# Kernel optimization log

Measured on AMD Instinct MI355X. Metric: run time of the kernel, lower is better.

Reference implementation:

```python
import jax, jax.numpy as jnp
import numpy as np

B, T, V, E, H = 64, 64, 32000, 512, 1024


def setup_inputs() -> dict:
    key = jax.random.key(0)
    ks = jax.random.split(key, 12)
    s = 0.02
    return {
        "hidden": jax.random.normal(ks[0], (2, B, H), jnp.float32),
        "cell": jax.random.normal(ks[1], (2, B, H), jnp.float32),
        "captions": jax.random.randint(ks[2], (B, T), 0, V, jnp.int32),
        "embed_W": jax.random.normal(ks[3], (V, E), jnp.float32) * s,
        "W_ih0": jax.random.normal(ks[4], (4 * H, E), jnp.float32) * s,
        "W_hh0": jax.random.normal(ks[5], (4 * H, H), jnp.float32) * s,
        "b_ih0": jnp.zeros((4 * H,), jnp.float32),
        "b_hh0": jnp.zeros((4 * H,), jnp.float32),
        "W_ih1": jax.random.normal(ks[6], (4 * H, H), jnp.float32) * s,
        "W_hh1": jax.random.normal(ks[7], (4 * H, H), jnp.float32) * s,
        "b_ih1": jnp.zeros((4 * H,), jnp.float32),
        "b_hh1": jnp.zeros((4 * H,), jnp.float32),
        "Wp_voc": jax.random.normal(ks[8], (V, H), jnp.float32) * s,
        "bp_voc": jnp.zeros((V,), jnp.float32),
    }


def lstm_cell(x, h, c, W_ih, W_hh, b):
    # PyTorch gate order: input, forget, cell(g), output
    gates = x @ W_ih.T + h @ W_hh.T + b  # [B, 4H]
    i, f, g, o = jnp.split(gates, 4, axis=-1)
    i, f, o = jax.nn.sigmoid(i), jax.nn.sigmoid(f), jax.nn.sigmoid(o)
    g = jnp.tanh(g)
    c_new = f * c + i * g
    h_new = o * jnp.tanh(c_new)
    return h_new, c_new


def reference(hidden, cell, captions, embed_W, W_ih0, W_hh0, b_ih0, b_hh0,
              W_ih1, W_hh1, b_ih1, b_hh1, Wp_voc, bp_voc):
    # teacher forcing (ratio=1.0): LSTM input at step t is embed(captions[:, t-1])
    x_seq = embed_W[captions[:, :-1]]        # [B, T-1, E]
    x_seq = jnp.swapaxes(x_seq, 0, 1)        # [T-1, B, E] time-major for scan
    b0 = b_ih0 + b_hh0
    b1 = b_ih1 + b_hh1

    def step(carry, x):
        h0, c0, h1, c1 = carry
        h0, c0 = lstm_cell(x, h0, c0, W_ih0, W_hh0, b0)
        h1, c1 = lstm_cell(h0, h1, c1, W_ih1, W_hh1, b1)
        logits = h1 @ Wp_voc.T + bp_voc      # [B, V]
        return (h0, c0, h1, c1), logits

    carry = (hidden[0], cell[0], hidden[1], cell[1])
    _, logits = jax.lax.scan(step, carry, x_seq)   # [T-1, B, V]
    logits = jnp.swapaxes(logits, 0, 1)            # [B, T-1, V]
    # outputs[:, 0, :] stays zero as in the torch code
    return jnp.concatenate([jnp.zeros((logits.shape[0], 1, logits.shape[2]), logits.dtype), logits], axis=1)
```

## Files before the change

kernel.cpp:

```cpp
#include <hip/hip_runtime.h>

#define B_    64
#define T_    64
#define V_    32000
#define E_    512
#define H_    1024
#define G4_   4096
#define TS_   63
#define MROWS 4032
#define MPAD  4096
#define BH    (B_ * H_)
#define FPAD  32

typedef __attribute__((ext_vector_type(8))) short bf16x8;
typedef __attribute__((ext_vector_type(4))) float f32x4;
typedef __attribute__((ext_vector_type(4))) unsigned int uint32x4;

__device__ __forceinline__ unsigned short bfbits(float f) {
  union { float f; unsigned int u; } cv; cv.f = f;
  unsigned int u = cv.u;
  u += 0x7fffu + ((u >> 16) & 1u);
  return (unsigned short)(u >> 16);
}
__device__ __forceinline__ float bf2f(unsigned short h) {
  union { unsigned int u; float f; } cv; cv.u = ((unsigned int)h) << 16;
  return cv.f;
}
__device__ __forceinline__ float fsig(float x) { return 1.f / (1.f + __expf(-x)); }
__device__ __forceinline__ float ftanh(float x) {
  x = fminf(fmaxf(x, -10.f), 10.f);
  const float e = __expf(2.f * x);
  return (e - 1.f) / (e + 1.f);
}

__device__ __forceinline__ void store_dword_dc(void* p, unsigned int v) {
  asm volatile("global_store_dword %0, %1, off sc0 sc1" :: "v"(p), "v"(v) : "memory");
}
__device__ __forceinline__ void store_b128_dc(void* p, uint32x4 v) {
  asm volatile("global_store_dwordx4 %0, %1, off sc0 sc1" :: "v"(p), "v"(v) : "memory");
}
__device__ __forceinline__ unsigned int load_dword_dc(const void* p) {
  unsigned int v;
  asm volatile("global_load_dword %0, %1, off sc0 sc1\n\ts_waitcnt vmcnt(0)"
               : "=v"(v) : "v"(p) : "memory");
  return v;
}
__device__ __forceinline__ void store_dword_nt(void* p, float f) {
  union { float f; unsigned int u; } cv; cv.f = f;
  asm volatile("global_store_dword %0, %1, off nt" :: "v"(p), "v"(cv.u) : "memory");
}

__device__ __forceinline__ void gload16(const void* g, void* l) {
  __builtin_amdgcn_global_load_lds(
      (const __attribute__((address_space(1))) unsigned int*)g,
      (__attribute__((address_space(3))) unsigned int*)l, 16, 0, 0);
}


__global__ void k_cast4(const float4* __restrict__ s, ushort4* __restrict__ d, int n4) {
  int i = blockIdx.x * blockDim.x + threadIdx.x;
  const int st = gridDim.x * blockDim.x;
  for (; i < n4; i += st) {
    const float4 f = s[i];
    ushort4 v;
    v.x = bfbits(f.x); v.y = bfbits(f.y); v.z = bfbits(f.z); v.w = bfbits(f.w);
    d[i] = v;
  }
}

__global__ void k_bias(const float* __restrict__ a, const float* __restrict__ b,
                       float* __restrict__ o, int n) {
  const int i = blockIdx.x * blockDim.x + threadIdx.x;
  if (i < n) o[i] = a[i] + b[i];
}

__global__ void k_gather(const float* __restrict__ embed, const int* __restrict__ caps,
                         unsigned short* __restrict__ X) {
  const int i = blockIdx.x * 256 + threadIdx.x;
  const int m = i >> 7, e4 = i & 127;
  ushort4 v;
  if (m < MROWS) {
    const int t = m >> 6, b = m & 63;
    const int idx = caps[b * T_ + t];
    const float4 f = ((const float4*)embed)[(long)idx * (E_ / 4) + e4];
    v.x = bfbits(f.x); v.y = bfbits(f.y); v.z = bfbits(f.z); v.w = bfbits(f.w);
  } else {
    v = make_ushort4(0, 0, 0, 0);
  }
  ((ushort4*)X)[i] = v;
}

__global__ void k_init(const float* __restrict__ hidden, const float* __restrict__ cell,
                       unsigned short* __restrict__ H0, unsigned short* __restrict__ H1,
                       float* __restrict__ c0, float* __restrict__ c1,
                       unsigned int* __restrict__ flags) {
  const int i = blockIdx.x * 256 + threadIdx.x;
  H0[i] = bfbits(hidden[i]);
  H1[i] = bfbits(hidden[B_ * H_ + i]);
  c0[i] = cell[i];
  c1[i] = cell[B_ * H_ + i];
  if (i < 192 * FPAD) flags[i] = 0u;
}

__global__ void k_zeropad(unsigned short* __restrict__ a, unsigned short* __restrict__ b) {
  const int i = blockIdx.x * 256 + threadIdx.x;
  a[i] = 0;
  b[i] = 0;
}

__global__ void k_zero_t0(float4* __restrict__ out4) {
  const int i = blockIdx.x * 256 + threadIdx.x;
  const int b = i / (V_ / 4), v = i - b * (V_ / 4);
  out4[(long)b * (T_ * V_ / 4) + v] = make_float4(0.f, 0.f, 0.f, 0.f);
}

__global__ __launch_bounds__(256) void k_gemm1(
    const unsigned short* __restrict__ A, const unsigned short* __restrict__ Bm,
    const float* __restrict__ bias, unsigned short* __restrict__ Cb) {
  __shared__ unsigned short As[128 * 32];
  __shared__ unsigned short Bs[128 * 32];
  const int tid = threadIdx.x;
  const int w = tid >> 6, l = tid & 63;
  const int wm = (w >> 1) * 64, wn = (w & 1) * 64;
  const int lr = l & 15, lk = (l >> 4) * 8;
  const long am0 = (long)blockIdx.y * 128;
  const long bn0 = (long)blockIdx.x * 128;

  const int u0 = tid, u1 = tid + 256;
  const char* gA0 = (const char*)(A + (am0 + (u0 >> 2)) * E_) + (u0 & 3) * 16;
  const char* gA1 = (const char*)(A + (am0 + (u1 >> 2)) * E_) + (u1 & 3) * 16;
  const char* gB0 = (const char*)(Bm + (bn0 + (u0 >> 2)) * E_) + (u0 & 3) * 16;
  const char* gB1 = (const char*)(Bm + (bn0 + (u1 >> 2)) * E_) + (u1 & 3) * 16;
  char* lA0 = (char*)As + u0 * 16; char* lA1 = (char*)As + u1 * 16;
  char* lB0 = (char*)Bs + u0 * 16; char* lB1 = (char*)Bs + u1 * 16;

  f32x4 acc[4][4];
  const f32x4 z = {0.f, 0.f, 0.f, 0.f};
  #pragma unroll
  for (int mi = 0; mi < 4; ++mi)
    #pragma unroll
    for (int ni = 0; ni < 4; ++ni) acc[mi][ni] = z;

  for (int k0 = 0; k0 < E_; k0 += 32) {
    __syncthreads();
    gload16(gA0 + (long)k0 * 2, lA0);
    gload16(gA1 + (long)k0 * 2, lA1);
    gload16(gB0 + (long)k0 * 2, lB0);
    gload16(gB1 + (long)k0 * 2, lB1);
    __syncthreads();
    bf16x8 af[4], bfr[4];
    #pragma unroll
    for (int mi = 0; mi < 4; ++mi)
      af[mi] = *(const bf16x8*)(As + (wm + mi * 16 + lr) * 32 + lk);
    #pragma unroll
    for (int ni = 0; ni < 4; ++ni)
      bfr[ni] = *(const bf16x8*)(Bs + (wn + ni * 16 + lr) * 32 + lk);
    #pragma unroll
    for (int mi = 0; mi < 4; ++mi)
      #pragma unroll
      for (int ni = 0; ni < 4; ++ni)
        acc[mi][ni] = __builtin_amdgcn_mfma_f32_16x16x32_bf16(af[mi], bfr[ni], acc[mi][ni], 0, 0, 0);
  }

  #pragma unroll
  for (int ni = 0; ni < 4; ++ni) {
    const int n = (int)bn0 + wn + ni * 16 + lr;
    const float bv = bias[n];
    #pragma unroll
    for (int mi = 0; mi < 4; ++mi) {
      #pragma unroll
      for (int r = 0; r < 4; ++r) {
        const int m = (int)am0 + wm + mi * 16 + (l >> 4) * 4 + r;
        Cb[(long)m * G4_ + n] = bfbits(acc[mi][ni][r] + bv);
      }
    }
  }
}

__global__ __launch_bounds__(512, 2) void k_gemm3(
    const unsigned short* __restrict__ A,
    const unsigned short* __restrict__ Bm,
    const float* __restrict__ bias,
    float* __restrict__ out) {
  __shared__ unsigned short As[2][256 * 64];
  __shared__ unsigned short Bs[2][256 * 64];
  const int tid = threadIdx.x;
  const int wid = tid >> 6, l = tid & 63;
  const int wr = wid >> 2, wc = wid & 3;
  const int lr = l & 15, khi = l >> 4;
  const int id = blockIdx.x;
  const int by = id / 125, bx = id - by * 125;
  const long am0 = (long)by * 256;
  const long bn0 = (long)bx * 256;

  int srow[4], sq[4];
  #pragma unroll
  for (int j = 0; j < 4; ++j) {
    const int idx = j * 512 + tid;
    srow[j] = idx >> 3;
    sq[j] = (idx & 7) ^ (srow[j] & 7);
  }

  f32x4 acc[8][4];
  const f32x4 z = {0.f, 0.f, 0.f, 0.f};
  #pragma unroll
  for (int mf = 0; mf < 8; ++mf)
    #pragma unroll
    for (int nf = 0; nf < 4; ++nf) acc[mf][nf] = z;

  auto stage = [&](int kt, int b) {
    const long koff = (long)kt * 128;
    #pragma unroll
    for (int j = 0; j < 4; ++j) {
      const int idx = j * 512 + tid;
      gload16((const char*)(A + (am0 + srow[j]) * H_) + koff + sq[j] * 16,
              (char*)As[b] + idx * 16);
    }
    #pragma unroll
    for (int j = 0; j < 4; ++j) {
      const int idx = j * 512 + tid;
      gload16((const char*)(Bm + (bn0 + srow[j]) * H_) + koff + sq[j] * 16,
              (char*)Bs[b] + idx * 16);
    }
  };

  stage(0, 0);
  for (int t = 0; t < 16; ++t) {
    const int c = t & 1;
    __builtin_amdgcn_s_barrier();
    if (t + 1 < 16) {
      stage(t + 1, c ^ 1);
      asm volatile("s_waitcnt vmcnt(8)" ::: "memory");
    } else {
      asm volatile("s_waitcnt vmcnt(0)" ::: "memory");
    }
    __builtin_amdgcn_s_barrier();
    #pragma unroll
    for (int ks = 0; ks < 2; ++ks) {
      const int qx = ((ks * 4 + khi) ^ (lr & 7)) * 16;
      bf16x8 af[8], bfr[4];
      #pragma unroll
      for (int mf = 0; mf < 8; ++mf) {
        const int row = wr * 128 + mf * 16 + lr;
        af[mf] = *(const bf16x8*)((const char*)As[c] + row * 128 + qx);
      }
      #pragma unroll
      for (int nf = 0; nf < 4; ++nf) {
        const int row = wc * 64 + nf * 16 + lr;
        bfr[nf] = *(const bf16x8*)((const char*)Bs[c] + row * 128 + qx);
      }
      __builtin_amdgcn_s_setprio(1);
      #pragma unroll
      for (int mf = 0; mf < 8; ++mf)
        #pragma unroll
        for (int nf = 0; nf < 4; ++nf)
          acc[mf][nf] = __builtin_amdgcn_mfma_f32_16x16x32_bf16(af[mf], bfr[nf], acc[mf][nf], 0, 0, 0);
      __builtin_amdgcn_s_setprio(0);
    }
  }

  #pragma unroll
  for (int nf = 0; nf < 4; ++nf) {
    const int n = (int)bn0 + wc * 64 + nf * 16 + lr;
    const float bv = bias[n];
    #pragma unroll
    for (int mf = 0; mf < 8; ++mf) {
      #pragma unroll
      for (int r = 0; r < 4; ++r) {
        const int m = (int)am0 + wr * 128 + mf * 16 + khi * 4 + r;
        if (m < MROWS) {
          const int t = m >> 6, b = m & 63;
          store_dword_nt(out + (long)(b * T_ + t + 1) * V_ + n, acc[mf][nf][r] + bv);
        }
      }
    }
  }
}

__global__ __launch_bounds__(256) void k_fused(
    const unsigned short* __restrict__ Whh0b,
    const unsigned short* __restrict__ Whh1b,
    const unsigned short* __restrict__ Wih1b,
    const unsigned short* __restrict__ Xp,
    unsigned short* __restrict__ H0b,
    unsigned short* __restrict__ H1b,
    const float* __restrict__ c0i, const float* __restrict__ c1i,
    const float* __restrict__ b1s,
    unsigned int* __restrict__ f0,
    unsigned int* __restrict__ f1) {
  __shared__ unsigned short Wl[64 * 1024];
  __shared__ __align__(16) float gs1[4][64][8];
  unsigned short (*hexch)[16] = (unsigned short (*)[16])gs1;

  const int tid = threadIdx.x;
  const int w = tid >> 6, l = tid & 63;
  const int lcol = l & 15, khi = l >> 4;
  const int bw = w * 16;
  const f32x4 z = {0.f, 0.f, 0.f, 0.f};

  if (blockIdx.x < 64) {
    const int blk = blockIdx.x;
    const int jb = blk << 4;
    for (int u = tid; u < 64 * 128; u += 256) {
      const int rr = u >> 7, cu = u & 127;
      const int g = rr >> 4, jj = rr & 15;
      ((bf16x8*)Wl)[rr * 128 + (cu ^ (rr & 7))] =
          *(const bf16x8*)(Whh0b + (size_t)(g * 1024 + jb + jj) * H_ + cu * 8);
    }
    f32x4 cr;
    #pragma unroll
    for (int r = 0; r < 4; ++r)
      cr[r] = c0i[(size_t)(bw + khi * 4 + r) * H_ + jb + lcol];
    unsigned short pin[16];
    #pragma unroll
    for (int r = 0; r < 4; ++r) {
      const unsigned short* ir = Xp + (size_t)(bw + khi * 4 + r) * G4_ + jb + lcol;
      pin[r * 4 + 0] = ir[0];
      pin[r * 4 + 1] = ir[H_];
      pin[r * 4 + 2] = ir[2 * H_];
      pin[r * 4 + 3] = ir[3 * H_];
    }
    __syncthreads();

    for (int s = 0; s < TS_; ++s) {
      if (s > 0) {
        if (tid < 64)
          while (load_dword_dc(&f0[tid << 5]) < (unsigned)s) __builtin_amdgcn_s_sleep(1);
        __syncthreads();
      }
      f32x4 a0, a1, a2, a3;
      #pragma unroll
      for (int r = 0; r < 4; ++r) {
        a0[r] = bf2f(pin[r * 4 + 0]);
        a1[r] = bf2f(pin[r * 4 + 1]);
        a2[r] = bf2f(pin[r * 4 + 2]);
        a3[r] = bf2f(pin[r * 4 + 3]);
      }
      const unsigned short* hrow = H0b + (size_t)s * BH + (size_t)(bw + lcol) * H_ + khi * 8;
      #pragma unroll 8
      for (int kk = 0; kk < 32; ++kk) {
        const bf16x8 av = *(const bf16x8*)(hrow + kk * 32);
        const int un = (kk * 4 + khi) ^ (lcol & 7);
        const bf16x8 b0 = ((const bf16x8*)Wl)[(0 * 16 + lcol) * 128 + un];
        const bf16x8 b1 = ((const bf16x8*)Wl)[(1 * 16 + lcol) * 128 + un];
        const bf16x8 b2 = ((const bf16x8*)Wl)[(2 * 16 + lcol) * 128 + un];
        const bf16x8 b3 = ((const bf16x8*)Wl)[(3 * 16 + lcol) * 128 + un];
        a0 = __builtin_amdgcn_mfma_f32_16x16x32_bf16(av, b0, a0, 0, 0, 0);
        a1 = __builtin_amdgcn_mfma_f32_16x16x32_bf16(av, b1, a1, 0, 0, 0);
        a2 = __builtin_amdgcn_mfma_f32_16x16x32_bf16(av, b2, a2, 0, 0, 0);
        a3 = __builtin_amdgcn_mfma_f32_16x16x32_bf16(av, b3, a3, 0, 0, 0);
      }
      #pragma unroll
      for (int r = 0; r < 4; ++r) {
        const float gi = fsig(a0[r]);
        const float gf = fsig(a1[r]);
        const float gg = ftanh(a2[r]);
        const float go = fsig(a3[r]);
        cr[r] = gf * cr[r] + gi * gg;
        hexch[bw + khi * 4 + r][lcol] = bfbits(go * ftanh(cr[r]));
      }
      if (s + 1 < TS_) {
        const unsigned short* inb = Xp + (size_t)(s + 1) * (B_ * G4_);
        #pragma unroll
        for (int r = 0; r < 4; ++r) {
          const unsigned short* ir = inb + (size_t)(bw + khi * 4 + r) * G4_ + jb + lcol;
          pin[r * 4 + 0] = ir[0];
          pin[r * 4 + 1] = ir[H_];
          pin[r * 4 + 2] = ir[2 * H_];
          pin[r * 4 + 3] = ir[3 * H_];
        }
      }
      __syncthreads();
      if (tid < 128) {
        const int b = tid >> 1, hf = tid & 1;
        const uint32x4 v = *(const uint32x4*)&hexch[b][hf * 8];
        store_b128_dc(H0b + (size_t)(s + 1) * BH + (size_t)b * H_ + jb + hf * 8, v);
      }
      __syncthreads();
      if (tid == 0) store_dword_dc(&f0[blk << 5], (unsigned)(s + 1));
    }
  } else {
    const int blk1 = blockIdx.x - 64;
    const int jb1 = blk1 << 3;
    for (int u = tid; u < 64 * 128; u += 256) {
      const int pr = u >> 7, cu = u & 127;
      const int prl = pr & 31, tt = prl >> 4, lr_ = prl & 15;
      const int g = tt * 2 + (lr_ >> 3), jj = lr_ & 7;
      const unsigned short* src =
          ((pr >> 5) ? Wih1b : Whh1b) + (size_t)(g * 1024 + jb1 + jj) * H_ + cu * 8;
      ((bf16x8*)Wl)[pr * 128 + (cu ^ (pr & 7))] = *(const bf16x8*)src;
    }
    const int bb = tid >> 2;
    const int j0 = (tid * 2) & 7;
    float cA = c1i[(size_t)bb * H_ + jb1 + j0];
    float cB = c1i[(size_t)bb * H_ + jb1 + j0 + 1];
    float biA[4], biB[4];
    #pragma unroll
    for (int g = 0; g < 4; ++g) {
      biA[g] = b1s[g * 1024 + jb1 + j0];
      biB[g] = b1s[g * 1024 + jb1 + j0 + 1];
    }
    __syncthreads();

    for (int s = 1; s <= TS_; ++s) {
      {
        const unsigned t0 = (unsigned)s, t1 = (unsigned)(s - 1);
        if (tid < 64) {
          while (load_dword_dc(&f0[tid << 5]) < t0) __builtin_amdgcn_s_sleep(1);
        } else if (tid < 192) {
          while (load_dword_dc(&f1[(tid - 64) << 5]) < t1) __builtin_amdgcn_s_sleep(1);
        }
        __syncthreads();
      }
      f32x4 ac0 = z, ac1 = z;
      const unsigned short* a1p = H1b + (size_t)(s - 1) * BH + (size_t)(bw + lcol) * H_ + khi * 8;
      const unsigned short* a0p = H0b + (size_t)s * BH + (size_t)(bw + lcol) * H_ + khi * 8;
      #pragma unroll 8
      for (int kk = 0; kk < 32; ++kk) {
        const bf16x8 av = *(const bf16x8*)(a1p + kk * 32);
        const int un = (kk * 4 + khi) ^ (lcol & 7);
        const bf16x8 b0 = ((const bf16x8*)Wl)[(0 + lcol) * 128 + un];
        const bf16x8 b1 = ((const bf16x8*)Wl)[(16 + lcol) * 128 + un];
        ac0 = __builtin_amdgcn_mfma_f32_16x16x32_bf16(av, b0, ac0, 0, 0, 0);
        ac1 = __builtin_amdgcn_mfma_f32_16x16x32_bf16(av, b1, ac1, 0, 0, 0);
      }
      #pragma unroll 8
      for (int kk = 0; kk < 32; ++kk) {
        const bf16x8 av = *(const bf16x8*)(a0p + kk * 32);
        const int un = (kk * 4 + khi) ^ (lcol & 7);
        const bf16x8 b0 = ((const bf16x8*)Wl)[(32 + lcol) * 128 + un];
        const bf16x8 b1 = ((const bf16x8*)Wl)[(48 + lcol) * 128 + un];
        ac0 = __builtin_amdgcn_mfma_f32_16x16x32_bf16(av, b0, ac0, 0, 0, 0);
        ac1 = __builtin_amdgcn_mfma_f32_16x16x32_bf16(av, b1, ac1, 0, 0, 0);
      }
      #pragma unroll
      for (int r = 0; r < 4; ++r) {
        const int b = bw + khi * 4 + r;
        gs1[lcol >> 3][b][lcol & 7] = ac0[r];
        gs1[2 + (lcol >> 3)][b][lcol & 7] = ac1[r];
      }
      __syncthreads();
      {
        const float giA = fsig(gs1[0][bb][j0] + biA[0]);
        const float gfA = fsig(gs1[1][bb][j0] + biA[1]);
        const float ggA = ftanh(gs1[2][bb][j0] + biA[2]);
        const float goA = fsig(gs1[3][bb][j0] + biA[3]);
        cA = gfA * cA + giA * ggA;
        const unsigned short hA = bfbits(goA * ftanh(cA));
        const float giB = fsig(gs1[0][bb][j0 + 1] + biB[0]);
        const float gfB = fsig(gs1[1][bb][j0 + 1] + biB[1]);
        const float ggB = ftanh(gs1[2][bb][j0 + 1] + biB[2]);
        const float goB = fsig(gs1[3][bb][j0 + 1] + biB[3]);
        cB = gfB * cB + giB * ggB;
        const unsigned short hB = bfbits(goB * ftanh(cB));
        const unsigned int hv = ((unsigned int)hB << 16) | hA;
        store_dword_dc(H1b + (size_t)s * BH + (size_t)bb * H_ + jb1 + j0, hv);
      }
      __syncthreads();
      if (tid == 0) store_dword_dc(&f1[blk1 << 5], (unsigned)s);
    }
  }
}


extern "C" void kernel_launch(void* const* d_in, const int* in_sizes, int n_in,
                              void* d_out, int out_size, void* d_ws, size_t ws_size,
                              hipStream_t stream) {
  (void)in_sizes; (void)n_in; (void)out_size; (void)ws_size;
  const float* hidden = (const float*)d_in[0];
  const float* cell   = (const float*)d_in[1];
  const int*   caps   = (const int*)d_in[2];
  const float* embed  = (const float*)d_in[3];
  const float* Wih0   = (const float*)d_in[4];
  const float* Whh0   = (const float*)d_in[5];
  const float* bih0   = (const float*)d_in[6];
  const float* bhh0   = (const float*)d_in[7];
  const float* Wih1   = (const float*)d_in[8];
  const float* Whh1   = (const float*)d_in[9];
  const float* bih1   = (const float*)d_in[10];
  const float* bhh1   = (const float*)d_in[11];
  const float* Wp     = (const float*)d_in[12];
  const float* bp     = (const float*)d_in[13];
  float* out = (float*)d_out;

  char* p = (char*)d_ws;
  auto alloc = [&](size_t bytes) { char* r = p; p += (bytes + 255) & ~(size_t)255; return r; };
  unsigned short* Xbf   = (unsigned short*)alloc((size_t)MPAD * E_ * 2);
  unsigned short* Wih0b = (unsigned short*)alloc((size_t)G4_ * E_ * 2);
  unsigned short* Whh0b = (unsigned short*)alloc((size_t)G4_ * H_ * 2);
  unsigned short* Wih1b = (unsigned short*)alloc((size_t)G4_ * H_ * 2);
  unsigned short* Whh1b = (unsigned short*)alloc((size_t)G4_ * H_ * 2);
  unsigned short* Wpb   = (unsigned short*)alloc((size_t)V_ * H_ * 2);
  unsigned short* Xp    = (unsigned short*)alloc((size_t)MPAD * G4_ * 2);
  unsigned short* H0    = (unsigned short*)alloc((size_t)(MPAD + B_) * H_ * 2);
  unsigned short* H1    = (unsigned short*)alloc((size_t)(MPAD + B_) * H_ * 2);
  float* c0  = (float*)alloc((size_t)B_ * H_ * 4);
  float* c1  = (float*)alloc((size_t)B_ * H_ * 4);
  float* b0s = (float*)alloc((size_t)G4_ * 4);
  float* b1s = (float*)alloc((size_t)G4_ * 4);
  unsigned int* cbar = (unsigned int*)alloc((size_t)192 * FPAD * 4);

  k_cast4<<<2048, 256, 0, stream>>>((const float4*)Wih0, (ushort4*)Wih0b, G4_ * E_ / 4);
  k_cast4<<<2048, 256, 0, stream>>>((const float4*)Whh0, (ushort4*)Whh0b, G4_ * H_ / 4);
  k_cast4<<<2048, 256, 0, stream>>>((const float4*)Wih1, (ushort4*)Wih1b, G4_ * H_ / 4);
  k_cast4<<<2048, 256, 0, stream>>>((const float4*)Whh1, (ushort4*)Whh1b, G4_ * H_ / 4);
  k_cast4<<<4096, 256, 0, stream>>>((const float4*)Wp,   (ushort4*)Wpb,   V_ * H_ / 4);
  k_bias<<<16, 256, 0, stream>>>(bih0, bhh0, b0s, G4_);
  k_bias<<<16, 256, 0, stream>>>(bih1, bhh1, b1s, G4_);
  k_gather<<<2048, 256, 0, stream>>>(embed, caps, Xbf);
  k_init<<<256, 256, 0, stream>>>(hidden, cell, H0, H1, c0, c1, cbar);
  k_zeropad<<<256, 256, 0, stream>>>(H0 + (size_t)MPAD * H_, H1 + (size_t)MPAD * H_);
  k_zero_t0<<<2000, 256, 0, stream>>>((float4*)out);

  k_gemm1<<<dim3(32, 32), 256, 0, stream>>>(Xbf, Wih0b, b0s, Xp);

  k_fused<<<192, 256, 0, stream>>>(Whh0b, Whh1b, Wih1b, Xp, H0, H1, c0, c1, b1s,
                                   cbar, cbar + 64 * FPAD);

  k_gemm3<<<2000, 512, 0, stream>>>(H1 + (size_t)B_ * H_, Wpb, bp, out);
}
```

Before: 1.047 ms.

## Merge setup kernels and switch vocab GEMM to three-stage K=32 pipeline

Combines the four LSTM weight casts into one kernel, the two bias sums into one, and the zero-padding into the init kernel, cutting the launch count. The vocab-projection GEMM now uses a triple-buffered LDS pipeline with half-size K tiles (32 instead of 64), a new swizzle and prefetch two stages ahead. Its LDS footprint drops and the launch-bounds occupancy hint is removed. The extra stage aims to hide global-load latency, at the cost of twice as many barriers per K.

```diff
diff --git a/kernel.cpp b/kernel.cpp
--- a/kernel.cpp
+++ b/kernel.cpp
@@ -68,10 +68,32 @@
   }
 }
 
-__global__ void k_bias(const float* __restrict__ a, const float* __restrict__ b,
-                       float* __restrict__ o, int n) {
-  const int i = blockIdx.x * blockDim.x + threadIdx.x;
-  if (i < n) o[i] = a[i] + b[i];
+__global__ void k_castW(const float4* __restrict__ s0, const float4* __restrict__ s1,
+                        const float4* __restrict__ s2, const float4* __restrict__ s3,
+                        ushort4* __restrict__ d0, ushort4* __restrict__ d1,
+                        ushort4* __restrict__ d2, ushort4* __restrict__ d3) {
+  const int N0 = G4_ * E_ / 4, N1 = G4_ * H_ / 4;
+  int i = blockIdx.x * 256 + threadIdx.x;
+  const int st = gridDim.x * 256;
+  for (; i < N0 + 3 * N1; i += st) {
+    const float4* s; ushort4* d; int k;
+    if (i < N0)            { s = s0; d = d0; k = i; }
+    else if (i < N0 + N1)  { s = s1; d = d1; k = i - N0; }
+    else if (i < N0 + 2*N1){ s = s2; d = d2; k = i - N0 - N1; }
+    else                   { s = s3; d = d3; k = i - N0 - 2 * N1; }
+    const float4 f = s[k];
+    ushort4 v;
+    v.x = bfbits(f.x); v.y = bfbits(f.y); v.z = bfbits(f.z); v.w = bfbits(f.w);
+    d[k] = v;
+  }
+}
+
+__global__ void k_bias2(const float* __restrict__ a0, const float* __restrict__ b0,
+                        const float* __restrict__ a1, const float* __restrict__ b1,
+                        float* __restrict__ o0, float* __restrict__ o1) {
+  const int i = blockIdx.x * 256 + threadIdx.x;
+  if (i < G4_) o0[i] = a0[i] + b0[i];
+  else         o1[i - G4_] = a1[i - G4_] + b1[i - G4_];
 }
 
 __global__ void k_gather(const float* __restrict__ embed, const int* __restrict__ caps,
@@ -95,17 +117,17 @@
                        float* __restrict__ c0, float* __restrict__ c1,
                        unsigned int* __restrict__ flags) {
   const int i = blockIdx.x * 256 + threadIdx.x;
-  H0[i] = bfbits(hidden[i]);
-  H1[i] = bfbits(hidden[B_ * H_ + i]);
-  c0[i] = cell[i];
-  c1[i] = cell[B_ * H_ + i];
-  if (i < 192 * FPAD) flags[i] = 0u;
-}
-
-__global__ void k_zeropad(unsigned short* __restrict__ a, unsigned short* __restrict__ b) {
-  const int i = blockIdx.x * 256 + threadIdx.x;
-  a[i] = 0;
-  b[i] = 0;
+  if (i < B_ * H_) {
+    H0[i] = bfbits(hidden[i]);
+    H1[i] = bfbits(hidden[B_ * H_ + i]);
+    c0[i] = cell[i];
+    c1[i] = cell[B_ * H_ + i];
+    if (i < 192 * FPAD) flags[i] = 0u;
+  } else {
+    const int j = i - B_ * H_;
+    H0[(size_t)MPAD * H_ + j] = 0;
+    H1[(size_t)MPAD * H_ + j] = 0;
+  }
 }
 
 __global__ void k_zero_t0(float4* __restrict__ out4) {
@@ -177,13 +199,13 @@
   }
 }
 
-__global__ __launch_bounds__(512, 2) void k_gemm3(
+__global__ __launch_bounds__(512) void k_gemm3(
     const unsigned short* __restrict__ A,
     const unsigned short* __restrict__ Bm,
     const float* __restrict__ bias,
     float* __restrict__ out) {
-  __shared__ unsigned short As[2][256 * 64];
-  __shared__ unsigned short Bs[2][256 * 64];
+  __shared__ unsigned short As[3][256 * 32];
+  __shared__ unsigned short Bs[3][256 * 32];
   const int tid = threadIdx.x;
   const int wid = tid >> 6, l = tid & 63;
   const int wr = wid >> 2, wc = wid & 3;
@@ -193,12 +215,12 @@
   const long am0 = (long)by * 256;
   const long bn0 = (long)bx * 256;
 
-  int srow[4], sq[4];
+  int srow[2], sq[2];
   #pragma unroll
-  for (int j = 0; j < 4; ++j) {
+  for (int j = 0; j < 2; ++j) {
     const int idx = j * 512 + tid;
-    srow[j] = idx >> 3;
-    sq[j] = (idx & 7) ^ (srow[j] & 7);
+    srow[j] = idx >> 2;
+    sq[j] = (idx & 3) ^ ((srow[j] >> 1) & 3);
   }
 
   f32x4 acc[8][4];
@@ -209,15 +231,15 @@
     for (int nf = 0; nf < 4; ++nf) acc[mf][nf] = z;
 
   auto stage = [&](int kt, int b) {
-    const long koff = (long)kt * 128;
-    #pragma unroll
-    for (int j = 0; j < 4; ++j) {
+    const long koff = (long)kt * 64;
+    #pragma unroll
+    for (int j = 0; j < 2; ++j) {
       const int idx = j * 512 + tid;
       gload16((const char*)(A + (am0 + srow[j]) * H_) + koff + sq[j] * 16,
               (char*)As[b] + idx * 16);
     }
     #pragma unroll
-    for (int j = 0; j < 4; ++j) {
+    for (int j = 0; j < 2; ++j) {
       const int idx = j * 512 + tid;
       gload16((const char*)(Bm + (bn0 + srow[j]) * H_) + koff + sq[j] * 16,
               (char*)Bs[b] + idx * 16);
@@ -225,38 +247,39 @@
   };
 
   stage(0, 0);
-  for (int t = 0; t < 16; ++t) {
-    const int c = t & 1;
+  stage(1, 1);
+  for (int t = 0; t < 32; ++t) {
+    const int c = t % 3;
     __builtin_amdgcn_s_barrier();
-    if (t + 1 < 16) {
-      stage(t + 1, c ^ 1);
+    if (t + 2 < 32) {
+      stage(t + 2, (t + 2) % 3);
       asm volatile("s_waitcnt vmcnt(8)" ::: "memory");
+    } else if (t + 1 < 32) {
+      asm volatile("s_waitcnt vmcnt(4)" ::: "memory");
     } else {
       asm volatile("s_waitcnt vmcnt(0)" ::: "memory");
     }
     __builtin_amdgcn_s_barrier();
-    #pragma unroll
-    for (int ks = 0; ks < 2; ++ks) {
-      const int qx = ((ks * 4 + khi) ^ (lr & 7)) * 16;
-      bf16x8 af[8], bfr[4];
-      #pragma unroll
-      for (int mf = 0; mf < 8; ++mf) {
-        const int row = wr * 128 + mf * 16 + lr;
-        af[mf] = *(const bf16x8*)((const char*)As[c] + row * 128 + qx);
-      }
-      #pragma unroll
-      for (int nf = 0; nf < 4; ++nf) {
-        const int row = wc * 64 + nf * 16 + lr;
-        bfr[nf] = *(const bf16x8*)((const char*)Bs[c] + row * 128 + qx);
-      }
-      __builtin_amdgcn_s_setprio(1);
-      #pragma unroll
-      for (int mf = 0; mf < 8; ++mf)
-        #pragma unroll
-        for (int nf = 0; nf < 4; ++nf)
-          acc[mf][nf] = __builtin_amdgcn_mfma_f32_16x16x32_bf16(af[mf], bfr[nf], acc[mf][nf], 0, 0, 0);
-      __builtin_amdgcn_s_setprio(0);
-    }
+    bf16x8 af[8], bfr[4];
+    #pragma unroll
+    for (int mf = 0; mf < 8; ++mf) {
+      const int row = wr * 128 + mf * 16 + lr;
+      const int q = khi ^ ((row >> 1) & 3);
+      af[mf] = *(const bf16x8*)((const char*)As[c] + row * 64 + q * 16);
+    }
+    #pragma unroll
+    for (int nf = 0; nf < 4; ++nf) {
+      const int row = wc * 64 + nf * 16 + lr;
+      const int q = khi ^ ((row >> 1) & 3);
+      bfr[nf] = *(const bf16x8*)((const char*)Bs[c] + row * 64 + q * 16);
+    }
+    __builtin_amdgcn_s_setprio(1);
+    #pragma unroll
+    for (int mf = 0; mf < 8; ++mf)
+      #pragma unroll
+      for (int nf = 0; nf < 4; ++nf)
+        acc[mf][nf] = __builtin_amdgcn_mfma_f32_16x16x32_bf16(af[mf], bfr[nf], acc[mf][nf], 0, 0, 0);
+    __builtin_amdgcn_s_setprio(0);
   }
 
   #pragma unroll
@@ -500,16 +523,14 @@
   float* b1s = (float*)alloc((size_t)G4_ * 4);
   unsigned int* cbar = (unsigned int*)alloc((size_t)192 * FPAD * 4);
 
-  k_cast4<<<2048, 256, 0, stream>>>((const float4*)Wih0, (ushort4*)Wih0b, G4_ * E_ / 4);
-  k_cast4<<<2048, 256, 0, stream>>>((const float4*)Whh0, (ushort4*)Whh0b, G4_ * H_ / 4);
-  k_cast4<<<2048, 256, 0, stream>>>((const float4*)Wih1, (ushort4*)Wih1b, G4_ * H_ / 4);
-  k_cast4<<<2048, 256, 0, stream>>>((const float4*)Whh1, (ushort4*)Whh1b, G4_ * H_ / 4);
-  k_cast4<<<4096, 256, 0, stream>>>((const float4*)Wp,   (ushort4*)Wpb,   V_ * H_ / 4);
-  k_bias<<<16, 256, 0, stream>>>(bih0, bhh0, b0s, G4_);
-  k_bias<<<16, 256, 0, stream>>>(bih1, bhh1, b1s, G4_);
+  k_castW<<<4096, 256, 0, stream>>>((const float4*)Wih0, (const float4*)Whh0,
+                                    (const float4*)Wih1, (const float4*)Whh1,
+                                    (ushort4*)Wih0b, (ushort4*)Whh0b,
+                                    (ushort4*)Wih1b, (ushort4*)Whh1b);
+  k_cast4<<<4096, 256, 0, stream>>>((const float4*)Wp, (ushort4*)Wpb, V_ * H_ / 4);
+  k_bias2<<<32, 256, 0, stream>>>(bih0, bhh0, bih1, bhh1, b0s, b1s);
   k_gather<<<2048, 256, 0, stream>>>(embed, caps, Xbf);
-  k_init<<<256, 256, 0, stream>>>(hidden, cell, H0, H1, c0, c1, cbar);
-  k_zeropad<<<256, 256, 0, stream>>>(H0 + (size_t)MPAD * H_, H1 + (size_t)MPAD * H_);
+  k_init<<<512, 256, 0, stream>>>(hidden, cell, H0, H1, c0, c1, cbar);
   k_zero_t0<<<2000, 256, 0, stream>>>((float4*)out);
 
   k_gemm1<<<dim3(32, 32), 256, 0, stream>>>(Xbf, Wih0b, b0s, Xp);
```

Result: slower. 1.085 ms (+3.7%).
